# Kernel tuning notes

Hardware: AMD Instinct MI355X
Metric: run time of the kernel (lower is better)

The kernel has to match this reference:

```python
import jax, jax.numpy as jnp
import numpy as np

N_NODES = 100000
N_EDGES = 600000
D_IN = 128
D_OUT = 128


def setup_inputs() -> dict:
    key = jax.random.key(0)
    ks = jax.random.split(key, 8)
    stdv = 1.0 / np.sqrt(D_OUT)
    return {
        "x": jax.random.normal(ks[0], (N_NODES, D_IN), dtype=jnp.float32),
        "edge_src": jax.random.randint(ks[1], (N_EDGES,), 0, N_NODES, dtype=jnp.int32),
        "edge_dst": jax.random.randint(ks[2], (N_EDGES,), 0, N_NODES, dtype=jnp.int32),
        "edge_weight": jax.random.uniform(ks[3], (N_EDGES,), dtype=jnp.float32),
        "weight_l": jax.random.uniform(ks[4], (D_IN, D_OUT), minval=-stdv, maxval=stdv, dtype=jnp.float32),
        "bias_l": jax.random.uniform(ks[5], (D_OUT,), minval=-stdv, maxval=stdv, dtype=jnp.float32),
        "weight_r": jax.random.uniform(ks[6], (D_IN, D_OUT), minval=-stdv, maxval=stdv, dtype=jnp.float32),
        "bias_r": jax.random.uniform(ks[7], (D_OUT,), minval=-stdv, maxval=stdv, dtype=jnp.float32),
    }


def reference(x, edge_src, edge_dst, edge_weight, weight_l, bias_l, weight_r, bias_r):
    # h = input @ weight_l  -> [N, D_OUT]
    h = x @ weight_l
    # spmm(adj, h): out[dst] += adj[dst, src] * h[src]
    msgs = h[edge_src] * edge_weight[:, None]          # [E, D_OUT] gather
    agg = jax.ops.segment_sum(msgs, edge_dst, num_segments=N_NODES)
    out = agg + bias_l
    # root_weight branch (size is None)
    out = out + x @ weight_r + bias_r
    return out
```

## Files before the change

### kernel.cpp

```cpp
#include <hip/hip_runtime.h>
#include <hip/hip_bf16.h>

#define D 128
#define SCAN_BLK 256
#define SCAN_VPT 4
#define SCAN_TILE (SCAN_BLK * SCAN_VPT)

typedef __attribute__((ext_vector_type(8))) short short8;
typedef __attribute__((ext_vector_type(4))) float f32x4;

__global__ __launch_bounds__(256) void prep_w(
    const float* __restrict__ Wl, const float* __restrict__ Wr,
    const float* __restrict__ bl, const float* __restrict__ br,
    __hip_bfloat16* __restrict__ WTl, __hip_bfloat16* __restrict__ WTr,
    float* __restrict__ bsum, int* __restrict__ deg,
    unsigned long long* __restrict__ state, int n_nodes) {
  const int tid = blockIdx.x * 256 + threadIdx.x;
  const int n = (tid >> 7) & 127;
  const int k = tid & 127;
  if (tid < 16384) {
    WTl[n * D + k] = __float2bfloat16(Wl[k * D + n]);
  } else {
    WTr[n * D + k] = __float2bfloat16(Wr[k * D + n]);
  }
  if (tid < 128) bsum[tid] = bl[tid] + br[tid];
  if (tid < 1024) state[tid] = 0ull;
  for (int i = tid; i < n_nodes; i += 32768) deg[i] = 0;
}

__global__ __launch_bounds__(256) void gemm_hr(
    const float* __restrict__ x, const __hip_bfloat16* __restrict__ WTl,
    const __hip_bfloat16* __restrict__ WTr, const float* __restrict__ bsum,
    __hip_bfloat16* __restrict__ h, float* __restrict__ out,
    const int* __restrict__ edst, int* __restrict__ deg, int n_edges,
    int n_rowtiles) {
  const int t = threadIdx.x;
  const int gsz = gridDim.x * 256;
  for (int e = blockIdx.x * 256 + t; e < n_edges; e += gsz)
    atomicAdd(&deg[edst[e]], 1);

  __shared__ __hip_bfloat16 xs[16][136];
  const int wave = t >> 6;
  const int lane = t & 63;
  const int m = lane & 15;
  const int q = lane >> 4;

  short8 bfl[2][4], bfr[2][4];
  float bias[2];
#pragma unroll
  for (int c = 0; c < 2; ++c) {
    const int n0 = wave * 32 + c * 16;
    bias[c] = bsum[n0 + m];
#pragma unroll
    for (int ks = 0; ks < 4; ++ks) {
      bfl[c][ks] = *(const short8*)&WTl[(n0 + m) * D + ks * 32 + q * 8];
      bfr[c][ks] = *(const short8*)&WTr[(n0 + m) * D + ks * 32 + q * 8];
    }
  }

  const int srow = t >> 4;
  const int scol = (t & 15) * 8;

  int rt = blockIdx.x;
  float4 pv0, pv1;
  if (rt < n_rowtiles) {
    const float4* src = (const float4*)&x[(size_t)(rt * 16 + srow) * D + scol];
    pv0 = src[0];
    pv1 = src[1];
  }

  for (; rt < n_rowtiles; rt += gridDim.x) {
    const int rowbase = rt * 16;

    {
      __hip_bfloat16* dst = &xs[srow][scol];
      dst[0] = __float2bfloat16(pv0.x); dst[1] = __float2bfloat16(pv0.y);
      dst[2] = __float2bfloat16(pv0.z); dst[3] = __float2bfloat16(pv0.w);
      dst[4] = __float2bfloat16(pv1.x); dst[5] = __float2bfloat16(pv1.y);
      dst[6] = __float2bfloat16(pv1.z); dst[7] = __float2bfloat16(pv1.w);
    }
    __syncthreads();

    const int nrt = rt + gridDim.x;
    if (nrt < n_rowtiles) {
      const float4* src = (const float4*)&x[(size_t)(nrt * 16 + srow) * D + scol];
      pv0 = src[0];
      pv1 = src[1];
    }

    f32x4 accL[2], accR[2];
#pragma unroll
    for (int c = 0; c < 2; ++c)
#pragma unroll
      for (int r = 0; r < 4; ++r) { accL[c][r] = 0.f; accR[c][r] = 0.f; }

#pragma unroll
    for (int ks = 0; ks < 4; ++ks) {
      const short8 afrag = *(const short8*)&xs[m][ks * 32 + q * 8];
#pragma unroll
      for (int c = 0; c < 2; ++c) {
        accL[c] = __builtin_amdgcn_mfma_f32_16x16x32_bf16(afrag, bfl[c][ks], accL[c], 0, 0, 0);
        accR[c] = __builtin_amdgcn_mfma_f32_16x16x32_bf16(afrag, bfr[c][ks], accR[c], 0, 0, 0);
      }
    }

#pragma unroll
    for (int c = 0; c < 2; ++c) {
      const int n = wave * 32 + c * 16 + m;
#pragma unroll
      for (int r = 0; r < 4; ++r) {
        const size_t row = (size_t)(rowbase + q * 4 + r);
        h[row * D + n] = __float2bfloat16(accL[c][r]);
        out[row * D + n] = accR[c][r] + bias[c];
      }
    }
    __syncthreads();
  }
}

__global__ __launch_bounds__(SCAN_BLK) void scan_ll(
    int* __restrict__ pos , int* __restrict__ offsets,
    unsigned long long* __restrict__ state, int n, int n_edges) {
  __shared__ int sdata[SCAN_BLK];
  __shared__ int s_prefix;
  const int t = threadIdx.x;
  const int b = blockIdx.x;
  const int base = b * SCAN_TILE + t * SCAN_VPT;

  int v[SCAN_VPT];
  int s = 0;
#pragma unroll
  for (int j = 0; j < SCAN_VPT; ++j) {
    v[j] = (base + j < n) ? pos[base + j] : 0;
    s += v[j];
  }
  sdata[t] = s;
  __syncthreads();
  for (int off = 1; off < SCAN_BLK; off <<= 1) {
    int xv = (t >= off) ? sdata[t - off] : 0;
    __syncthreads();
    sdata[t] += xv;
    __syncthreads();
  }
  const int excl = sdata[t] - s;
  const int total = sdata[SCAN_BLK - 1];

  if (t == 0) {
    const unsigned long long st =
        ((unsigned long long)(b == 0 ? 2 : 1) << 62) | (unsigned int)total;
    __hip_atomic_store(&state[b], st, __ATOMIC_RELEASE, __HIP_MEMORY_SCOPE_AGENT);
  }

  if (b == 0) {
    if (t == 0) s_prefix = 0;
  } else if (t < 64) {
    int windowEnd = b;
    int acc = 0;
    for (;;) {
      const int j = windowEnd - 1 - t;
      unsigned long long st = 0;
      if (j >= 0) {
        do {
          st = __hip_atomic_load(&state[j], __ATOMIC_ACQUIRE, __HIP_MEMORY_SCOPE_AGENT);
        } while (st == 0);
      }
      const int flag = (j >= 0) ? (int)(st >> 62) : 2;
      const int val = (j >= 0) ? (int)(st & 0xffffffffull) : 0;
      const unsigned long long mask = __ballot(flag == 2);
      if (mask) {
        const int firstLane = __ffsll((long long)mask) - 1;
        int contrib = (t <= firstLane) ? val : 0;
#pragma unroll
        for (int o = 32; o > 0; o >>= 1) contrib += __shfl_down(contrib, o);
        if (t == 0) { acc += contrib; s_prefix = acc; }
        break;
      } else {
        int contrib = val;
#pragma unroll
        for (int o = 32; o > 0; o >>= 1) contrib += __shfl_down(contrib, o);
        if (t == 0) acc += contrib;
        windowEnd -= 64;
      }
    }
  }
  __syncthreads();
  const int add = s_prefix;

  if (t == 0 && b > 0) {
    const unsigned long long st = (2ull << 62) | (unsigned int)(add + total);
    __hip_atomic_store(&state[b], st, __ATOMIC_RELEASE, __HIP_MEMORY_SCOPE_AGENT);
  }

  int run = add + excl;
#pragma unroll
  for (int j = 0; j < SCAN_VPT; ++j) {
    if (base + j < n) {
      offsets[base + j] = run;
      pos[base + j] = run;
    }
    run += v[j];
  }
  if (b == 0 && t == 0) offsets[n] = n_edges;
}

__global__ __launch_bounds__(256) void scatter_kernel(
    const int* __restrict__ esrc, const int* __restrict__ edst,
    const float* __restrict__ ew, int* __restrict__ pos,
    int2* __restrict__ pairs, int n_edges) {
  const int e = blockIdx.x * 256 + threadIdx.x;
  if (e >= n_edges) return;
  const int d = edst[e];
  const int slot = atomicAdd(&pos[d], 1);
  pairs[slot] = make_int2(esrc[e], __float_as_int(ew[e]));
}

__global__ __launch_bounds__(256) void sage_agg(
    const __hip_bfloat16* __restrict__ h,
    const int* __restrict__ offsets, const int2* __restrict__ pairs,
    float* __restrict__ out, int n_nodes) {
  const int node = blockIdx.x * 4 + (threadIdx.x >> 6);
  const int lane = threadIdx.x & 63;
  if (node >= n_nodes) return;
  const int begin = offsets[node];
  const int end = offsets[node + 1];
  const __hip_bfloat162* __restrict__ h2 = (const __hip_bfloat162*)h;

  float2 a = *(const float2*)&out[(size_t)node * D + 2 * lane];

  int i = begin;
  for (; i + 8 <= end; i += 8) {
    int2 p[8];
#pragma unroll
    for (int u = 0; u < 8; ++u) p[u] = pairs[i + u];
    __hip_bfloat162 hv[8];
#pragma unroll
    for (int u = 0; u < 8; ++u)
      hv[u] = h2[(size_t)p[u].x * (D / 2) + lane];
#pragma unroll
    for (int u = 0; u < 8; ++u) {
      const float w = __int_as_float(p[u].y);
      a.x = fmaf(w, __bfloat162float(hv[u].x), a.x);
      a.y = fmaf(w, __bfloat162float(hv[u].y), a.y);
    }
  }
  if (i < end) {
    int2 p[8];
#pragma unroll
    for (int u = 0; u < 8; ++u) {
      const int ei = (i + u < end) ? (i + u) : (end - 1);
      p[u] = pairs[ei];
      if (i + u >= end) p[u].y = 0;
    }
    __hip_bfloat162 hv[8];
#pragma unroll
    for (int u = 0; u < 8; ++u)
      hv[u] = h2[(size_t)p[u].x * (D / 2) + lane];
#pragma unroll
    for (int u = 0; u < 8; ++u) {
      const float w = __int_as_float(p[u].y);
      a.x = fmaf(w, __bfloat162float(hv[u].x), a.x);
      a.y = fmaf(w, __bfloat162float(hv[u].y), a.y);
    }
  }

  *(float2*)&out[(size_t)node * D + 2 * lane] = a;
}

extern "C" void kernel_launch(void* const* d_in, const int* in_sizes, int n_in,
                              void* d_out, int out_size, void* d_ws, size_t ws_size,
                              hipStream_t stream) {
  const float* x   = (const float*)d_in[0];
  const int* esrc  = (const int*)d_in[1];
  const int* edst  = (const int*)d_in[2];
  const float* ew  = (const float*)d_in[3];
  const float* Wl  = (const float*)d_in[4];
  const float* bl  = (const float*)d_in[5];
  const float* Wr  = (const float*)d_in[6];
  const float* br  = (const float*)d_in[7];
  float* out = (float*)d_out;

  const int n_nodes = in_sizes[0] / D;
  const int n_edges = in_sizes[1];

  char* ws = (char*)d_ws;
  size_t off = 0;
  __hip_bfloat16* h = (__hip_bfloat16*)(ws + off);
  off += (size_t)n_nodes * D * sizeof(__hip_bfloat16);
  off = (off + 15) & ~15ull;
  int* offsets = (int*)(ws + off);
  off += (size_t)(n_nodes + 1) * sizeof(int);
  off = (off + 15) & ~15ull;
  int* pos = (int*)(ws + off);
  off += (size_t)n_nodes * sizeof(int);
  off = (off + 15) & ~15ull;
  unsigned long long* state = (unsigned long long*)(ws + off);
  off += 1024 * sizeof(unsigned long long);
  off = (off + 15) & ~15ull;
  int2* pairs = (int2*)(ws + off);
  off += (size_t)n_edges * sizeof(int2);
  off = (off + 15) & ~15ull;
  __hip_bfloat16* WTl = (__hip_bfloat16*)(ws + off);
  off += (size_t)D * D * sizeof(__hip_bfloat16);
  __hip_bfloat16* WTr = (__hip_bfloat16*)(ws + off);
  off += (size_t)D * D * sizeof(__hip_bfloat16);
  float* bsum = (float*)(ws + off);
  off += D * sizeof(float);

  prep_w<<<128, 256, 0, stream>>>(Wl, Wr, bl, br, WTl, WTr, bsum, pos, state, n_nodes);

  const int n_rowtiles = (n_nodes + 15) / 16;
  const int gemm_grid = n_rowtiles < 2048 ? n_rowtiles : 2048;
  gemm_hr<<<gemm_grid, 256, 0, stream>>>(x, WTl, WTr, bsum, h, out, edst, pos,
                                         n_edges, n_rowtiles);

  const int nparts = (n_nodes + SCAN_TILE - 1) / SCAN_TILE;
  scan_ll<<<nparts, SCAN_BLK, 0, stream>>>(pos, offsets, state, n_nodes, n_edges);

  scatter_kernel<<<(n_edges + 255) / 256, 256, 0, stream>>>(esrc, edst, ew, pos, pairs, n_edges);

  sage_agg<<<(n_nodes + 3) / 4, 256, 0, stream>>>(h, offsets, pairs, out, n_nodes);
}
```

Before: 242.6 us.

## Move degree counting into prep kernel, memset counters, one-tile-per-block GEMM

The edge-degree atomic histogram moves from the GEMM kernel into the weight-prep kernel, which now launches 512 blocks. Zeroing of the degree counters and scan state is replaced by a single hipMemsetAsync. The GEMM drops its persistent grid-stride loop and register prefetch, launching one block per 16-row tile instead. This separates the atomic-bound and MFMA-bound phases and removes the loop overhead, but it gives up the prefetch overlap and adds a memset launch.

```diff
diff --git a/kernel.cpp b/kernel.cpp
--- a/kernel.cpp
+++ b/kernel.cpp
@@ -13,37 +13,36 @@
     const float* __restrict__ Wl, const float* __restrict__ Wr,
     const float* __restrict__ bl, const float* __restrict__ br,
     __hip_bfloat16* __restrict__ WTl, __hip_bfloat16* __restrict__ WTr,
-    float* __restrict__ bsum, int* __restrict__ deg,
-    unsigned long long* __restrict__ state, int n_nodes) {
+    float* __restrict__ bsum,
+    const int* __restrict__ edst, int* __restrict__ deg, int n_edges) {
   const int tid = blockIdx.x * 256 + threadIdx.x;
-  const int n = (tid >> 7) & 127;
-  const int k = tid & 127;
   if (tid < 16384) {
+    const int n = (tid >> 7) & 127;
+    const int k = tid & 127;
     WTl[n * D + k] = __float2bfloat16(Wl[k * D + n]);
-  } else {
+  } else if (tid < 32768) {
+    const int n = (tid >> 7) & 127;
+    const int k = tid & 127;
     WTr[n * D + k] = __float2bfloat16(Wr[k * D + n]);
   }
   if (tid < 128) bsum[tid] = bl[tid] + br[tid];
-  if (tid < 1024) state[tid] = 0ull;
-  for (int i = tid; i < n_nodes; i += 32768) deg[i] = 0;
+
+  const int gsz = gridDim.x * 256;
+  for (int e = tid; e < n_edges; e += gsz)
+    atomicAdd(&deg[edst[e]], 1);
 }
 
 __global__ __launch_bounds__(256) void gemm_hr(
     const float* __restrict__ x, const __hip_bfloat16* __restrict__ WTl,
     const __hip_bfloat16* __restrict__ WTr, const float* __restrict__ bsum,
-    __hip_bfloat16* __restrict__ h, float* __restrict__ out,
-    const int* __restrict__ edst, int* __restrict__ deg, int n_edges,
-    int n_rowtiles) {
+    __hip_bfloat16* __restrict__ h, float* __restrict__ out) {
+  __shared__ __hip_bfloat16 xs[16][136];
   const int t = threadIdx.x;
-  const int gsz = gridDim.x * 256;
-  for (int e = blockIdx.x * 256 + t; e < n_edges; e += gsz)
-    atomicAdd(&deg[edst[e]], 1);
-
-  __shared__ __hip_bfloat16 xs[16][136];
   const int wave = t >> 6;
   const int lane = t & 63;
   const int m = lane & 15;
   const int q = lane >> 4;
+  const int rowbase = blockIdx.x * 16;
 
   short8 bfl[2][4], bfr[2][4];
   float bias[2];
@@ -58,63 +57,44 @@
     }
   }
 
-  const int srow = t >> 4;
-  const int scol = (t & 15) * 8;
-
-  int rt = blockIdx.x;
-  float4 pv0, pv1;
-  if (rt < n_rowtiles) {
-    const float4* src = (const float4*)&x[(size_t)(rt * 16 + srow) * D + scol];
-    pv0 = src[0];
-    pv1 = src[1];
-  }
-
-  for (; rt < n_rowtiles; rt += gridDim.x) {
-    const int rowbase = rt * 16;
-
-    {
-      __hip_bfloat16* dst = &xs[srow][scol];
-      dst[0] = __float2bfloat16(pv0.x); dst[1] = __float2bfloat16(pv0.y);
-      dst[2] = __float2bfloat16(pv0.z); dst[3] = __float2bfloat16(pv0.w);
-      dst[4] = __float2bfloat16(pv1.x); dst[5] = __float2bfloat16(pv1.y);
-      dst[6] = __float2bfloat16(pv1.z); dst[7] = __float2bfloat16(pv1.w);
-    }
-    __syncthreads();
-
-    const int nrt = rt + gridDim.x;
-    if (nrt < n_rowtiles) {
-      const float4* src = (const float4*)&x[(size_t)(nrt * 16 + srow) * D + scol];
-      pv0 = src[0];
-      pv1 = src[1];
-    }
-
-    f32x4 accL[2], accR[2];
-#pragma unroll
-    for (int c = 0; c < 2; ++c)
-#pragma unroll
-      for (int r = 0; r < 4; ++r) { accL[c][r] = 0.f; accR[c][r] = 0.f; }
-
-#pragma unroll
-    for (int ks = 0; ks < 4; ++ks) {
-      const short8 afrag = *(const short8*)&xs[m][ks * 32 + q * 8];
-#pragma unroll
-      for (int c = 0; c < 2; ++c) {
-        accL[c] = __builtin_amdgcn_mfma_f32_16x16x32_bf16(afrag, bfl[c][ks], accL[c], 0, 0, 0);
-        accR[c] = __builtin_amdgcn_mfma_f32_16x16x32_bf16(afrag, bfr[c][ks], accR[c], 0, 0, 0);
-      }
-    }
-
+  {
+    const int srow = t >> 4;
+    const int scol = (t & 15) * 8;
+    const float4* src = (const float4*)&x[(size_t)(rowbase + srow) * D + scol];
+    const float4 v0 = src[0], v1 = src[1];
+    __hip_bfloat16* dst = &xs[srow][scol];
+    dst[0] = __float2bfloat16(v0.x); dst[1] = __float2bfloat16(v0.y);
+    dst[2] = __float2bfloat16(v0.z); dst[3] = __float2bfloat16(v0.w);
+    dst[4] = __float2bfloat16(v1.x); dst[5] = __float2bfloat16(v1.y);
+    dst[6] = __float2bfloat16(v1.z); dst[7] = __float2bfloat16(v1.w);
+  }
+  __syncthreads();
+
+  f32x4 accL[2], accR[2];
+#pragma unroll
+  for (int c = 0; c < 2; ++c)
+#pragma unroll
+    for (int r = 0; r < 4; ++r) { accL[c][r] = 0.f; accR[c][r] = 0.f; }
+
+#pragma unroll
+  for (int ks = 0; ks < 4; ++ks) {
+    const short8 afrag = *(const short8*)&xs[m][ks * 32 + q * 8];
 #pragma unroll
     for (int c = 0; c < 2; ++c) {
-      const int n = wave * 32 + c * 16 + m;
-#pragma unroll
-      for (int r = 0; r < 4; ++r) {
-        const size_t row = (size_t)(rowbase + q * 4 + r);
-        h[row * D + n] = __float2bfloat16(accL[c][r]);
-        out[row * D + n] = accR[c][r] + bias[c];
-      }
-    }
-    __syncthreads();
+      accL[c] = __builtin_amdgcn_mfma_f32_16x16x32_bf16(afrag, bfl[c][ks], accL[c], 0, 0, 0);
+      accR[c] = __builtin_amdgcn_mfma_f32_16x16x32_bf16(afrag, bfr[c][ks], accR[c], 0, 0, 0);
+    }
+  }
+
+#pragma unroll
+  for (int c = 0; c < 2; ++c) {
+    const int n = wave * 32 + c * 16 + m;
+#pragma unroll
+    for (int r = 0; r < 4; ++r) {
+      const size_t row = (size_t)(rowbase + q * 4 + r);
+      h[row * D + n] = __float2bfloat16(accL[c][r]);
+      out[row * D + n] = accR[c][r] + bias[c];
+    }
   }
 }
 
@@ -291,10 +271,12 @@
   off += (size_t)(n_nodes + 1) * sizeof(int);
   off = (off + 15) & ~15ull;
   int* pos = (int*)(ws + off);
+  size_t pos_off = off;
   off += (size_t)n_nodes * sizeof(int);
   off = (off + 15) & ~15ull;
   unsigned long long* state = (unsigned long long*)(ws + off);
   off += 1024 * sizeof(unsigned long long);
+  size_t zero_bytes = off - pos_off;
   off = (off + 15) & ~15ull;
   int2* pairs = (int2*)(ws + off);
   off += (size_t)n_edges * sizeof(int2);
@@ -306,12 +288,12 @@
   float* bsum = (float*)(ws + off);
   off += D * sizeof(float);
 
-  prep_w<<<128, 256, 0, stream>>>(Wl, Wr, bl, br, WTl, WTr, bsum, pos, state, n_nodes);
+  hipMemsetAsync(pos, 0, zero_bytes, stream);
+
+  prep_w<<<512, 256, 0, stream>>>(Wl, Wr, bl, br, WTl, WTr, bsum, edst, pos, n_edges);
 
   const int n_rowtiles = (n_nodes + 15) / 16;
-  const int gemm_grid = n_rowtiles < 2048 ? n_rowtiles : 2048;
-  gemm_hr<<<gemm_grid, 256, 0, stream>>>(x, WTl, WTr, bsum, h, out, edst, pos,
-                                         n_edges, n_rowtiles);
+  gemm_hr<<<n_rowtiles, 256, 0, stream>>>(x, WTl, WTr, bsum, h, out);
 
   const int nparts = (n_nodes + SCAN_TILE - 1) / SCAN_TILE;
   scan_ll<<<nparts, SCAN_BLK, 0, stream>>>(pos, offsets, state, n_nodes, n_edges);
```

After: 274.5 us. 1.13x slower.
